# Kernel tuning notes

Hardware: AMD Instinct MI355X
Metric: run time of the kernel (lower is better)

## Reference

```python
import jax, jax.numpy as jnp
import numpy as np

D = 512
E = 1024
LAMBDA_INIT = 0.05

def setup_inputs() -> dict:
    key = jax.random.key(0)
    ks = jax.random.split(key, 8)
    B, S = 4, 4096
    X = jax.random.normal(ks[0], (B, S, E), dtype=jnp.float32)
    Wq = jax.random.normal(ks[1], (2 * D, E), dtype=jnp.float32) / np.sqrt(E)
    bq = jnp.zeros((2 * D,), dtype=jnp.float32)
    Wk = jax.random.normal(ks[2], (2 * D, E), dtype=jnp.float32) / np.sqrt(E)
    bk = jnp.zeros((2 * D,), dtype=jnp.float32)
    Wv = jax.random.normal(ks[3], (D, E), dtype=jnp.float32) / np.sqrt(E)
    bv = jnp.zeros((D,), dtype=jnp.float32)
    lam = jax.random.normal(ks[4], (1,), dtype=jnp.float32)
    return {"X": X, "Wq": Wq, "bq": bq, "Wk": Wk, "bk": bk, "Wv": Wv, "bv": bv, "lam": lam}

def reference(X, Wq, bq, Wk, bk, Wv, bv, lam):
    # Linear projections (torch Linear: x @ W.T + b)
    Q = jnp.einsum('bse,fe->bsf', X, Wq) + bq   # [B,S,2d]
    K = jnp.einsum('bse,fe->bsf', X, Wk) + bk   # [B,S,2d]
    V = jnp.einsum('bse,de->bsd', X, Wv) + bv   # [B,S,d]
    Q1, Q2 = Q[..., :D], Q[..., D:]
    K1, K2 = K[..., :D], K[..., D:]
    s = 1.0 / np.sqrt(D)
    A1 = jnp.einsum('bqd,bkd->bqk', Q1, K1) * s  # [B,S,S]
    A2 = jnp.einsum('bqd,bkd->bqk', Q2, K2) * s
    P1 = jax.nn.softmax(A1, axis=-1)
    P2 = jax.nn.softmax(A2, axis=-1)
    lambda_ = jnp.exp(lam) + LAMBDA_INIT         # scalar [1]
    diff = P1 - lambda_ * P2
    return jnp.einsum('bqk,bkd->bqd', diff, V)   # [B,S,d]
```

## Files before the change

kernel.cpp:

```cpp
#include <hip/hip_runtime.h>
#include <cstdint>
#include <cstddef>

#define NB    4
#define SEQ   4096
#define EDIM  1024
#define DHEAD 512
#define NTOK  (NB * SEQ)
#define FQK   2048
#define FQKV  2560

typedef __bf16 bf16x8 __attribute__((ext_vector_type(8)));
typedef float  f32x4  __attribute__((ext_vector_type(4)));

__device__ __forceinline__ unsigned short f2bf(float f) {
  union { float f; unsigned int u; } v; v.f = f;
  return (unsigned short)((v.u + 0x7fffu + ((v.u >> 16) & 1u)) >> 16);
}
__device__ __forceinline__ float bf2f(unsigned short h) {
  union { unsigned int u; float f; } v; v.u = ((unsigned int)h) << 16;
  return v.f;
}

__device__ __forceinline__ void gld_lds16(const void* g, void* l) {
  __builtin_amdgcn_global_load_lds(
      (const __attribute__((address_space(1))) unsigned int*)g,
      (__attribute__((address_space(3))) unsigned int*)l, 16, 0, 0);
}

template <class Epi>
__device__ __forceinline__ void gemm_bt_core(
    const unsigned short* __restrict__ A, const unsigned short* __restrict__ B,
    int K, int lda, int ldb, int m0, int n0, Epi epi) {
  __shared__ __align__(16) unsigned short As[2][128 * 32];
  __shared__ __align__(16) unsigned short Bs[2][128 * 32];
  const int t = threadIdx.x;
  const int w = t >> 6;
  const int lane = t & 63;
  const int wr = w >> 1, wc = w & 1;

  f32x4 acc[4][4];
#pragma unroll
  for (int i = 0; i < 4; ++i)
#pragma unroll
    for (int j = 0; j < 4; ++j) acc[i][j] = f32x4{0.f, 0.f, 0.f, 0.f};

  const int c0 = (w * 2) * 64 + lane;
  const int c1 = (w * 2 + 1) * 64 + lane;
  const int r0 = c0 >> 2, col0 = (c0 & 3) * 8;
  const int r1 = c1 >> 2, col1 = (c1 & 3) * 8;
  const int o0 = (w * 2) * 512;
  const int o1 = (w * 2 + 1) * 512;
  const unsigned short* gA0 = A + (size_t)(m0 + r0) * lda + col0;
  const unsigned short* gA1 = A + (size_t)(m0 + r1) * lda + col1;
  const unsigned short* gB0 = B + (size_t)(n0 + r0) * ldb + col0;
  const unsigned short* gB1 = B + (size_t)(n0 + r1) * ldb + col1;

  gld_lds16(gA0, &As[0][o0]);
  gld_lds16(gA1, &As[0][o1]);
  gld_lds16(gB0, &Bs[0][o0]);
  gld_lds16(gB1, &Bs[0][o1]);
  __syncthreads();

  int cur = 0;
  for (int kt = 0; kt < K; kt += 32) {
    const int nxt = cur ^ 1;
    if (kt + 32 < K) {
      gld_lds16(gA0 + kt + 32, &As[nxt][o0]);
      gld_lds16(gA1 + kt + 32, &As[nxt][o1]);
      gld_lds16(gB0 + kt + 32, &Bs[nxt][o0]);
      gld_lds16(gB1 + kt + 32, &Bs[nxt][o1]);
    }
    bf16x8 af[4], bfr[4];
#pragma unroll
    for (int tm = 0; tm < 4; ++tm) {
      int r = wr * 64 + tm * 16 + (lane & 15);
      af[tm] = *(const bf16x8*)&As[cur][r * 32 + (lane >> 4) * 8];
    }
#pragma unroll
    for (int tn = 0; tn < 4; ++tn) {
      int r = wc * 64 + tn * 16 + (lane & 15);
      bfr[tn] = *(const bf16x8*)&Bs[cur][r * 32 + (lane >> 4) * 8];
    }
#pragma unroll
    for (int tm = 0; tm < 4; ++tm)
#pragma unroll
      for (int tn = 0; tn < 4; ++tn)
        acc[tm][tn] = __builtin_amdgcn_mfma_f32_16x16x32_bf16(
            af[tm], bfr[tn], acc[tm][tn], 0, 0, 0);
    __syncthreads();
    cur = nxt;
  }
  epi(acc, wr, wc, lane);
}

__global__ void k_cvt_x(const float* __restrict__ X, unsigned short* __restrict__ Xb) {
  int i = blockIdx.x * blockDim.x + threadIdx.x;
  float4 v = ((const float4*)X)[i];
  ushort4 o;
  o.x = f2bf(v.x); o.y = f2bf(v.y); o.z = f2bf(v.z); o.w = f2bf(v.w);
  ((ushort4*)Xb)[i] = o;
}

__global__ void k_pack_w(const float* __restrict__ Wq, const float* __restrict__ Wk,
                         const float* __restrict__ Wv, unsigned short* __restrict__ Wb) {
  int i = blockIdx.x * blockDim.x + threadIdx.x;
  int idx = i * 4;
  int f = idx >> 10, e = idx & 1023;
  const float* src = (f < 1024) ? (Wq + (size_t)f * 1024)
                   : (f < 2048) ? (Wk + (size_t)(f - 1024) * 1024)
                                : (Wv + (size_t)(f - 2048) * 1024);
  float4 v = *(const float4*)(src + e);
  ushort4 o;
  o.x = f2bf(v.x); o.y = f2bf(v.y); o.z = f2bf(v.z); o.w = f2bf(v.w);
  ((ushort4*)Wb)[i] = o;
}

__global__ void k_pack_b(const float* __restrict__ bq, const float* __restrict__ bk,
                         const float* __restrict__ bv, float* __restrict__ bc) {
  int f = blockIdx.x * blockDim.x + threadIdx.x;
  if (f < FQKV)
    bc[f] = (f < 1024) ? bq[f] : (f < 2048) ? bk[f - 1024] : bv[f - 2048];
}

__global__ void k_zero_f(float* __restrict__ p) {
  int i = blockIdx.x * blockDim.x + threadIdx.x;
  p[i] = 0.f;
}

__global__ __launch_bounds__(256) void k_qk(const unsigned short* __restrict__ Xb,
                                            const unsigned short* __restrict__ Wb,
                                            const float* __restrict__ bc,
                                            unsigned short* __restrict__ QK) {
  const int m0 = blockIdx.y * 128, n0 = blockIdx.x * 128;
  gemm_bt_core(Xb, Wb, EDIM, EDIM, EDIM, m0, n0,
    [&](f32x4 (&acc)[4][4], int wr, int wc, int lane) {
#pragma unroll
      for (int tm = 0; tm < 4; ++tm)
#pragma unroll
        for (int tn = 0; tn < 4; ++tn) {
          int kc = n0 + wc * 64 + tn * 16 + (lane & 15);
          float bias = bc[kc];
#pragma unroll
          for (int i = 0; i < 4; ++i) {
            int q = m0 + wr * 64 + tm * 16 + (lane >> 4) * 4 + i;
            QK[(size_t)q * FQK + kc] = f2bf(acc[tm][tn][i] + bias);
          }
        }
    });
}

__global__ __launch_bounds__(256) void k_v(const unsigned short* __restrict__ Xb,
                                           const unsigned short* __restrict__ Wb,
                                           const float* __restrict__ bc,
                                           unsigned short* __restrict__ Vt) {
  const int b = blockIdx.z;
  const int m0 = blockIdx.y * 128;
  const int n0 = blockIdx.x * 128;
  const unsigned short* A = Wb + (size_t)2048 * EDIM;
  const unsigned short* B = Xb + (size_t)b * SEQ * EDIM;
  unsigned short* Vb = Vt + (size_t)b * DHEAD * SEQ;
  gemm_bt_core(A, B, EDIM, EDIM, EDIM, m0, n0,
    [&](f32x4 (&acc)[4][4], int wr, int wc, int lane) {
#pragma unroll
      for (int tm = 0; tm < 4; ++tm)
#pragma unroll
        for (int tn = 0; tn < 4; ++tn) {
          int s = n0 + wc * 64 + tn * 16 + (lane & 15);
#pragma unroll
          for (int i = 0; i < 4; ++i) {
            int d = m0 + wr * 64 + tm * 16 + (lane >> 4) * 4 + i;
            Vb[(size_t)d * SEQ + s] = f2bf(acc[tm][tn][i] + bc[2048 + d]);
          }
        }
    });
}

__global__ __launch_bounds__(512) void k_scores3(const unsigned short* __restrict__ QK,
                                                 unsigned short* __restrict__ E_c,
                                                 float* __restrict__ ls, int b0) {
  __shared__ __align__(16) unsigned short As[2][256 * 32];
  __shared__ __align__(16) unsigned short Bs[2][128 * 32];
  const int z = blockIdx.z;
  const int rb = z >> 1, which = z & 1;
  const int b = b0 + rb;
  const int m0 = blockIdx.y * 256;
  const int n0 = blockIdx.x * 128;
  const unsigned short* Aq = QK + (size_t)b * SEQ * FQK + which * 512;
  const unsigned short* Bk = QK + (size_t)b * SEQ * FQK + 1024 + which * 512;
  unsigned short* Eb = E_c + (size_t)z * SEQ * SEQ;
  float* lr = ls + (size_t)which * NTOK + (size_t)b * SEQ;
  const int t = threadIdx.x, w = t >> 6, lane = t & 63;
  const int wr = w >> 1, wc = w & 1;

  f32x4 acc[4][4];
#pragma unroll
  for (int i = 0; i < 4; ++i)
#pragma unroll
    for (int j = 0; j < 4; ++j) acc[i][j] = f32x4{0.f, 0.f, 0.f, 0.f};

  const int cA0 = w * 128 + lane;
  const int cA1 = w * 128 + 64 + lane;
  const int cB  = w * 64 + lane;
  const unsigned short* gA0 = Aq + (size_t)(m0 + (cA0 >> 2)) * FQK + (cA0 & 3) * 8;
  const unsigned short* gA1 = Aq + (size_t)(m0 + (cA1 >> 2)) * FQK + (cA1 & 3) * 8;
  const unsigned short* gB  = Bk + (size_t)(n0 + (cB >> 2)) * FQK + (cB & 3) * 8;
  const int oA0 = (w * 128) * 8;
  const int oA1 = (w * 128 + 64) * 8;
  const int oB  = (w * 64) * 8;

  gld_lds16(gA0, &As[0][oA0]);
  gld_lds16(gA1, &As[0][oA1]);
  gld_lds16(gB,  &Bs[0][oB]);
  __syncthreads();

  int cur = 0;
  for (int kt = 0; kt < 512; kt += 32) {
    const int nxt = cur ^ 1;
    if (kt + 32 < 512) {
      gld_lds16(gA0 + kt + 32, &As[nxt][oA0]);
      gld_lds16(gA1 + kt + 32, &As[nxt][oA1]);
      gld_lds16(gB + kt + 32,  &Bs[nxt][oB]);
    }
    bf16x8 af[4], bfr[4];
#pragma unroll
    for (int tm = 0; tm < 4; ++tm) {
      int r = wr * 64 + tm * 16 + (lane & 15);
      af[tm] = *(const bf16x8*)&As[cur][r * 32 + (lane >> 4) * 8];
    }
#pragma unroll
    for (int tn = 0; tn < 4; ++tn) {
      int r = wc * 64 + tn * 16 + (lane & 15);
      bfr[tn] = *(const bf16x8*)&Bs[cur][r * 32 + (lane >> 4) * 8];
    }
#pragma unroll
    for (int tm = 0; tm < 4; ++tm)
#pragma unroll
      for (int tn = 0; tn < 4; ++tn)
        acc[tm][tn] = __builtin_amdgcn_mfma_f32_16x16x32_bf16(
            af[tm], bfr[tn], acc[tm][tn], 0, 0, 0);
    __syncthreads();
    cur = nxt;
  }

  const float scale = 0.04419417382415922f;
  float rs[4][4];
#pragma unroll
  for (int tm = 0; tm < 4; ++tm)
#pragma unroll
    for (int i = 0; i < 4; ++i) rs[tm][i] = 0.f;
#pragma unroll
  for (int tm = 0; tm < 4; ++tm)
#pragma unroll
    for (int tn = 0; tn < 4; ++tn) {
      int k = n0 + wc * 64 + tn * 16 + (lane & 15);
#pragma unroll
      for (int i = 0; i < 4; ++i) {
        int q = m0 + wr * 64 + tm * 16 + (lane >> 4) * 4 + i;
        float e = __expf(acc[tm][tn][i] * scale);
        unsigned short eb = f2bf(e);
        Eb[(size_t)q * SEQ + k] = eb;
        rs[tm][i] += bf2f(eb);
      }
    }
#pragma unroll
  for (int tm = 0; tm < 4; ++tm)
#pragma unroll
    for (int i = 0; i < 4; ++i) {
      float v = rs[tm][i];
      v += __shfl_xor(v, 1);
      v += __shfl_xor(v, 2);
      v += __shfl_xor(v, 4);
      v += __shfl_xor(v, 8);
      rs[tm][i] = v;
    }
  if ((lane & 15) == 0) {
#pragma unroll
    for (int tm = 0; tm < 4; ++tm)
#pragma unroll
      for (int i = 0; i < 4; ++i) {
        int q = m0 + wr * 64 + tm * 16 + (lane >> 4) * 4 + i;
        atomicAdd(&lr[q], rs[tm][i]);
      }
  }
}

__global__ __launch_bounds__(256) void k_pv4(const unsigned short* __restrict__ E_c,
                                             const unsigned short* __restrict__ Vt,
                                             float* __restrict__ O12, int b0) {
  __shared__ __align__(16) unsigned short As[2][64 * 32];
  __shared__ __align__(16) unsigned short Bs[2][256 * 32];
  const int bid = blockIdx.x;
  const int z = (bid >> 1) & 3;
  const int e = (bid & 1) | ((bid >> 3) << 1);
  const int q0 = (e >> 1) * 64;
  const int n0 = (e & 1) * 256;
  const int b = b0 + (z >> 1);
  const unsigned short* A = E_c + (size_t)z * SEQ * SEQ;
  const unsigned short* Bv = Vt + (size_t)b * DHEAD * SEQ;
  float* Ob = O12 + (size_t)z * SEQ * DHEAD;
  const int t = threadIdx.x, w = t >> 6, lane = t & 63;

  f32x4 acc[4][4];
#pragma unroll
  for (int i = 0; i < 4; ++i)
#pragma unroll
    for (int j = 0; j < 4; ++j) acc[i][j] = f32x4{0.f, 0.f, 0.f, 0.f};

  const int ca = w * 64 + lane;
  const unsigned short* gA = A + (size_t)(q0 + (ca >> 2)) * SEQ + (ca & 3) * 8;
  const int oA = (w * 64) * 8;
  const unsigned short* gB[4];
  int oB[4];
#pragma unroll
  for (int g = 0; g < 4; ++g) {
    int c = w * 256 + g * 64 + lane;
    gB[g] = Bv + (size_t)(n0 + (c >> 2)) * SEQ + (c & 3) * 8;
    oB[g] = (w * 256 + g * 64) * 8;
  }

  gld_lds16(gA, &As[0][oA]);
#pragma unroll
  for (int g = 0; g < 4; ++g) gld_lds16(gB[g], &Bs[0][oB[g]]);
  __syncthreads();

  int cur = 0;
  for (int kt = 0; kt < SEQ; kt += 32) {
    const int nxt = cur ^ 1;
    if (kt + 32 < SEQ) {
      gld_lds16(gA + kt + 32, &As[nxt][oA]);
#pragma unroll
      for (int g = 0; g < 4; ++g) gld_lds16(gB[g] + kt + 32, &Bs[nxt][oB[g]]);
    }
    bf16x8 af[4], bfr[4];
#pragma unroll
    for (int tm = 0; tm < 4; ++tm) {
      int r = tm * 16 + (lane & 15);
      af[tm] = *(const bf16x8*)&As[cur][r * 32 + (lane >> 4) * 8];
    }
#pragma unroll
    for (int tn = 0; tn < 4; ++tn) {
      int r = w * 64 + tn * 16 + (lane & 15);
      bfr[tn] = *(const bf16x8*)&Bs[cur][r * 32 + (lane >> 4) * 8];
    }
#pragma unroll
    for (int tm = 0; tm < 4; ++tm)
#pragma unroll
      for (int tn = 0; tn < 4; ++tn)
        acc[tm][tn] = __builtin_amdgcn_mfma_f32_16x16x32_bf16(
            af[tm], bfr[tn], acc[tm][tn], 0, 0, 0);
    __syncthreads();
    cur = nxt;
  }

#pragma unroll
  for (int tm = 0; tm < 4; ++tm)
#pragma unroll
    for (int tn = 0; tn < 4; ++tn) {
      int d = n0 + w * 64 + tn * 16 + (lane & 15);
#pragma unroll
      for (int i = 0; i < 4; ++i) {
        int q = q0 + tm * 16 + (lane >> 4) * 4 + i;
        Ob[(size_t)q * DHEAD + d] = acc[tm][tn][i];
      }
    }
}

__global__ void k_combine(const float* __restrict__ O12, const float* __restrict__ ls,
                          const float* __restrict__ lam, float* __restrict__ out, int b0) {
  int i = blockIdx.x * blockDim.x + threadIdx.x;
  float lambda = expf(lam[0]) + 0.05f;
  int gq = i >> 7;
  int rb = gq >> 12;
  int q = gq & 4095;
  int dv = i & 127;
  int b = b0 + rb;
  float inv1 = 1.f / ls[(size_t)b * SEQ + q];
  float inv2 = lambda / ls[NTOK + (size_t)b * SEQ + q];
  size_t ai = (size_t)(rb * 2) * (SEQ * 128) + (size_t)q * 128 + dv;
  float4 a = ((const float4*)O12)[ai];
  float4 c = ((const float4*)O12)[ai + SEQ * 128];
  float4 r;
  r.x = a.x * inv1 - c.x * inv2;
  r.y = a.y * inv1 - c.y * inv2;
  r.z = a.z * inv1 - c.z * inv2;
  r.w = a.w * inv1 - c.w * inv2;
  ((float4*)out)[(size_t)(b * SEQ + q) * 128 + dv] = r;
}

extern "C" void kernel_launch(void* const* d_in, const int* in_sizes, int n_in,
                              void* d_out, int out_size, void* d_ws, size_t ws_size,
                              hipStream_t stream) {
  const float* X   = (const float*)d_in[0];
  const float* Wq  = (const float*)d_in[1];
  const float* bq  = (const float*)d_in[2];
  const float* Wk  = (const float*)d_in[3];
  const float* bk  = (const float*)d_in[4];
  const float* Wv  = (const float*)d_in[5];
  const float* bv  = (const float*)d_in[6];
  const float* lam = (const float*)d_in[7];
  float* out = (float*)d_out;

  char* ws = (char*)d_ws;
  size_t off = 0;
  auto alloc = [&](size_t b) { size_t r = off; off += (b + 255) & ~(size_t)255; return r; };
  unsigned short* Xb  = (unsigned short*)(ws + alloc((size_t)NTOK * EDIM * 2));
  unsigned short* Wb  = (unsigned short*)(ws + alloc((size_t)FQKV * EDIM * 2));
  float*          bc  = (float*)(ws + alloc((size_t)FQKV * 4));
  unsigned short* QK  = (unsigned short*)(ws + alloc((size_t)NTOK * FQK * 2));
  unsigned short* Vt  = (unsigned short*)(ws + alloc((size_t)NB * DHEAD * SEQ * 2));
  unsigned short* E_c = (unsigned short*)(ws + alloc((size_t)4 * SEQ * SEQ * 2));
  float*          ls  = (float*)(ws + alloc((size_t)2 * NTOK * 4));
  float* O12 = (float*)Xb;

  k_cvt_x<<<dim3((NTOK * EDIM / 4) / 256), dim3(256), 0, stream>>>(X, Xb);
  k_pack_w<<<dim3((FQKV * EDIM / 4) / 256), dim3(256), 0, stream>>>(Wq, Wk, Wv, Wb);
  k_pack_b<<<dim3(10), dim3(256), 0, stream>>>(bq, bk, bv, bc);
  k_qk<<<dim3(FQK / 128, NTOK / 128), dim3(256), 0, stream>>>(Xb, Wb, bc, QK);
  k_v<<<dim3(SEQ / 128, DHEAD / 128, NB), dim3(256), 0, stream>>>(Xb, Wb, bc, Vt);
  k_zero_f<<<dim3(2 * NTOK / 256), dim3(256), 0, stream>>>(ls);
  for (int b0 = 0; b0 < NB; b0 += 2) {
    k_scores3<<<dim3(SEQ / 128, SEQ / 256, 4), dim3(512), 0, stream>>>(QK, E_c, ls, b0);
    k_pv4<<<dim3(512), dim3(256), 0, stream>>>(E_c, Vt, O12, b0);
    k_combine<<<dim3((2 * SEQ * DHEAD / 4) / 256), dim3(256), 0, stream>>>(O12, ls, lam, out, b0);
  }

  (void)in_sizes; (void)n_in; (void)out_size; (void)ws_size;
}
```

Baseline: 719.9 us.

## Triple-buffer LDS staging with partial vmcnt waits in all GEMM kernels

Moves the three GEMM-style kernels (generic projection GEMM, scores, PV) from double to triple buffering of their LDS tiles. Global-to-LDS loads are issued two tiles ahead, and each step waits only on the older tile's loads through an explicit s_waitcnt vmcnt(N) and a raw barrier instead of a full __syncthreads. The goal is to keep more memory traffic in flight and hide load latency behind MFMA work. The cost is 1.5x LDS per block, which may reduce occupancy, and a reliance on hand-counted vmcnt values being correct.

```diff
diff --git a/kernel.cpp b/kernel.cpp
--- a/kernel.cpp
+++ b/kernel.cpp
@@ -13,6 +13,9 @@
 typedef __bf16 bf16x8 __attribute__((ext_vector_type(8)));
 typedef float  f32x4  __attribute__((ext_vector_type(4)));
 
+#define WAITCNT(VM) asm volatile("s_waitcnt vmcnt(" #VM ") lgkmcnt(0)" ::: "memory")
+#define BAR() __builtin_amdgcn_s_barrier()
+
 __device__ __forceinline__ unsigned short f2bf(float f) {
   union { float f; unsigned int u; } v; v.f = f;
   return (unsigned short)((v.u + 0x7fffu + ((v.u >> 16) & 1u)) >> 16);
@@ -32,8 +35,8 @@
 __device__ __forceinline__ void gemm_bt_core(
     const unsigned short* __restrict__ A, const unsigned short* __restrict__ B,
     int K, int lda, int ldb, int m0, int n0, Epi epi) {
-  __shared__ __align__(16) unsigned short As[2][128 * 32];
-  __shared__ __align__(16) unsigned short Bs[2][128 * 32];
+  __shared__ __align__(16) unsigned short As[3][128 * 32];
+  __shared__ __align__(16) unsigned short Bs[3][128 * 32];
   const int t = threadIdx.x;
   const int w = t >> 6;
   const int lane = t & 63;
@@ -56,20 +59,25 @@
   const unsigned short* gB0 = B + (size_t)(n0 + r0) * ldb + col0;
   const unsigned short* gB1 = B + (size_t)(n0 + r1) * ldb + col1;
 
-  gld_lds16(gA0, &As[0][o0]);
-  gld_lds16(gA1, &As[0][o1]);
-  gld_lds16(gB0, &Bs[0][o0]);
-  gld_lds16(gB1, &Bs[0][o1]);
-  __syncthreads();
+  auto stage = [&](int buf, int tt) {
+    const int kt = tt * 32;
+    gld_lds16(gA0 + kt, &As[buf][o0]);
+    gld_lds16(gA1 + kt, &As[buf][o1]);
+    gld_lds16(gB0 + kt, &Bs[buf][o0]);
+    gld_lds16(gB1 + kt, &Bs[buf][o1]);
+  };
+
+  const int NT = K >> 5;
+  stage(0, 0);
+  stage(1, 1);
+  WAITCNT(4);
+  BAR();
 
   int cur = 0;
-  for (int kt = 0; kt < K; kt += 32) {
-    const int nxt = cur ^ 1;
-    if (kt + 32 < K) {
-      gld_lds16(gA0 + kt + 32, &As[nxt][o0]);
-      gld_lds16(gA1 + kt + 32, &As[nxt][o1]);
-      gld_lds16(gB0 + kt + 32, &Bs[nxt][o0]);
-      gld_lds16(gB1 + kt + 32, &Bs[nxt][o1]);
+  for (int tt = 0; tt < NT; ++tt) {
+    if (tt + 2 < NT) {
+      const int sb = (cur >= 1) ? cur - 1 : 2;
+      stage(sb, tt + 2);
     }
     bf16x8 af[4], bfr[4];
 #pragma unroll
@@ -88,8 +96,9 @@
       for (int tn = 0; tn < 4; ++tn)
         acc[tm][tn] = __builtin_amdgcn_mfma_f32_16x16x32_bf16(
             af[tm], bfr[tn], acc[tm][tn], 0, 0, 0);
-    __syncthreads();
-    cur = nxt;
+    if (tt < NT - 2)       { WAITCNT(4); BAR(); }
+    else if (tt == NT - 2) { WAITCNT(0); BAR(); }
+    cur = (cur == 2) ? 0 : cur + 1;
   }
   epi(acc, wr, wc, lane);
 }
@@ -179,8 +188,8 @@
 __global__ __launch_bounds__(512) void k_scores3(const unsigned short* __restrict__ QK,
                                                  unsigned short* __restrict__ E_c,
                                                  float* __restrict__ ls, int b0) {
-  __shared__ __align__(16) unsigned short As[2][256 * 32];
-  __shared__ __align__(16) unsigned short Bs[2][128 * 32];
+  __shared__ __align__(16) unsigned short As[3][256 * 32];
+  __shared__ __align__(16) unsigned short Bs[3][128 * 32];
   const int z = blockIdx.z;
   const int rb = z >> 1, which = z & 1;
   const int b = b0 + rb;
@@ -209,18 +218,24 @@
   const int oA1 = (w * 128 + 64) * 8;
   const int oB  = (w * 64) * 8;
 
-  gld_lds16(gA0, &As[0][oA0]);
-  gld_lds16(gA1, &As[0][oA1]);
-  gld_lds16(gB,  &Bs[0][oB]);
-  __syncthreads();
+  auto stage = [&](int buf, int tt) {
+    const int kt = tt * 32;
+    gld_lds16(gA0 + kt, &As[buf][oA0]);
+    gld_lds16(gA1 + kt, &As[buf][oA1]);
+    gld_lds16(gB + kt,  &Bs[buf][oB]);
+  };
+
+  const int NT = 16;
+  stage(0, 0);
+  stage(1, 1);
+  WAITCNT(3);
+  BAR();
 
   int cur = 0;
-  for (int kt = 0; kt < 512; kt += 32) {
-    const int nxt = cur ^ 1;
-    if (kt + 32 < 512) {
-      gld_lds16(gA0 + kt + 32, &As[nxt][oA0]);
-      gld_lds16(gA1 + kt + 32, &As[nxt][oA1]);
-      gld_lds16(gB + kt + 32,  &Bs[nxt][oB]);
+  for (int tt = 0; tt < NT; ++tt) {
+    if (tt + 2 < NT) {
+      const int sb = (cur >= 1) ? cur - 1 : 2;
+      stage(sb, tt + 2);
     }
     bf16x8 af[4], bfr[4];
 #pragma unroll
@@ -239,8 +254,9 @@
       for (int tn = 0; tn < 4; ++tn)
         acc[tm][tn] = __builtin_amdgcn_mfma_f32_16x16x32_bf16(
             af[tm], bfr[tn], acc[tm][tn], 0, 0, 0);
-    __syncthreads();
-    cur = nxt;
+    if (tt < NT - 2)       { WAITCNT(3); BAR(); }
+    else if (tt == NT - 2) { WAITCNT(0); BAR(); }
+    cur = (cur == 2) ? 0 : cur + 1;
   }
 
   const float scale = 0.04419417382415922f;
@@ -288,8 +304,8 @@
 __global__ __launch_bounds__(256) void k_pv4(const unsigned short* __restrict__ E_c,
                                              const unsigned short* __restrict__ Vt,
                                              float* __restrict__ O12, int b0) {
-  __shared__ __align__(16) unsigned short As[2][64 * 32];
-  __shared__ __align__(16) unsigned short Bs[2][256 * 32];
+  __shared__ __align__(16) unsigned short As[3][64 * 32];
+  __shared__ __align__(16) unsigned short Bs[3][256 * 32];
   const int bid = blockIdx.x;
   const int z = (bid >> 1) & 3;
   const int e = (bid & 1) | ((bid >> 3) << 1);
@@ -319,18 +335,24 @@
     oB[g] = (w * 256 + g * 64) * 8;
   }
 
-  gld_lds16(gA, &As[0][oA]);
-#pragma unroll
-  for (int g = 0; g < 4; ++g) gld_lds16(gB[g], &Bs[0][oB[g]]);
-  __syncthreads();
+  auto stage = [&](int buf, int tt) {
+    const int kt = tt * 32;
+    gld_lds16(gA + kt, &As[buf][oA]);
+#pragma unroll
+    for (int g = 0; g < 4; ++g) gld_lds16(gB[g] + kt, &Bs[buf][oB[g]]);
+  };
+
+  const int NT = SEQ / 32;
+  stage(0, 0);
+  stage(1, 1);
+  WAITCNT(5);
+  BAR();
 
   int cur = 0;
-  for (int kt = 0; kt < SEQ; kt += 32) {
-    const int nxt = cur ^ 1;
-    if (kt + 32 < SEQ) {
-      gld_lds16(gA + kt + 32, &As[nxt][oA]);
-#pragma unroll
-      for (int g = 0; g < 4; ++g) gld_lds16(gB[g] + kt + 32, &Bs[nxt][oB[g]]);
+  for (int tt = 0; tt < NT; ++tt) {
+    if (tt + 2 < NT) {
+      const int sb = (cur >= 1) ? cur - 1 : 2;
+      stage(sb, tt + 2);
     }
     bf16x8 af[4], bfr[4];
 #pragma unroll
@@ -349,8 +371,9 @@
       for (int tn = 0; tn < 4; ++tn)
         acc[tm][tn] = __builtin_amdgcn_mfma_f32_16x16x32_bf16(
             af[tm], bfr[tn], acc[tm][tn], 0, 0, 0);
-    __syncthreads();
-    cur = nxt;
+    if (tt < NT - 2)       { WAITCNT(5); BAR(); }
+    else if (tt == NT - 2) { WAITCNT(0); BAR(); }
+    cur = (cur == 2) ? 0 : cur + 1;
   }
 
 #pragma unroll
```

Result: slower. 807.1 us (+12.1%).

## Enlarge score and PV GEMM tiles with XOR-swizzled LDS and K=64 stages

Applied to the files above, without the earlier changes.

Both the score GEMM and the PV GEMM now use larger 256-wide tiles, 512 threads and a K step of 64 per LDS stage. Stage columns are XOR-swizzled to avoid LDS bank conflicts, and s_setprio raises wave priority around the MFMA section. PV blocks move from 64x256 to 256x128 tiles on a 3D grid, which changes how much E and V each block reuses. The cost is more LDS and registers per block (launch bounds 512,2), which may reduce occupancy.

```diff
diff --git a/kernel.cpp b/kernel.cpp
--- a/kernel.cpp
+++ b/kernel.cpp
@@ -176,87 +176,95 @@
     });
 }
 
-__global__ __launch_bounds__(512) void k_scores3(const unsigned short* __restrict__ QK,
-                                                 unsigned short* __restrict__ E_c,
-                                                 float* __restrict__ ls, int b0) {
-  __shared__ __align__(16) unsigned short As[2][256 * 32];
-  __shared__ __align__(16) unsigned short Bs[2][128 * 32];
-  const int z = blockIdx.z;
-  const int rb = z >> 1, which = z & 1;
-  const int b = b0 + rb;
-  const int m0 = blockIdx.y * 256;
-  const int n0 = blockIdx.x * 128;
+__global__ __launch_bounds__(512, 2) void k_scores8(const unsigned short* __restrict__ QK,
+                                                    unsigned short* __restrict__ E_c,
+                                                    float* __restrict__ ls, int b0) {
+  __shared__ __align__(16) unsigned short LA[2][256 * 64];
+  __shared__ __align__(16) unsigned short LB[2][256 * 64];
+  const int z = blockIdx.z, rb = z >> 1, which = z & 1, b = b0 + rb;
+  const int m0 = blockIdx.y * 256, n0 = blockIdx.x * 256;
   const unsigned short* Aq = QK + (size_t)b * SEQ * FQK + which * 512;
-  const unsigned short* Bk = QK + (size_t)b * SEQ * FQK + 1024 + which * 512;
+  const unsigned short* Bk = Aq + 1024;
   unsigned short* Eb = E_c + (size_t)z * SEQ * SEQ;
   float* lr = ls + (size_t)which * NTOK + (size_t)b * SEQ;
   const int t = threadIdx.x, w = t >> 6, lane = t & 63;
-  const int wr = w >> 1, wc = w & 1;
-
-  f32x4 acc[4][4];
-#pragma unroll
-  for (int i = 0; i < 4; ++i)
+  const int wr = w >> 2, wc = w & 3;
+  const int l15 = lane & 15, c16 = lane >> 4, x7 = l15 & 7;
+
+  f32x4 acc[8][4];
+#pragma unroll
+  for (int i = 0; i < 8; ++i)
 #pragma unroll
     for (int j = 0; j < 4; ++j) acc[i][j] = f32x4{0.f, 0.f, 0.f, 0.f};
 
-  const int cA0 = w * 128 + lane;
-  const int cA1 = w * 128 + 64 + lane;
-  const int cB  = w * 64 + lane;
-  const unsigned short* gA0 = Aq + (size_t)(m0 + (cA0 >> 2)) * FQK + (cA0 & 3) * 8;
-  const unsigned short* gA1 = Aq + (size_t)(m0 + (cA1 >> 2)) * FQK + (cA1 & 3) * 8;
-  const unsigned short* gB  = Bk + (size_t)(n0 + (cB >> 2)) * FQK + (cB & 3) * 8;
-  const int oA0 = (w * 128) * 8;
-  const int oA1 = (w * 128 + 64) * 8;
-  const int oB  = (w * 64) * 8;
-
-  gld_lds16(gA0, &As[0][oA0]);
-  gld_lds16(gA1, &As[0][oA1]);
-  gld_lds16(gB,  &Bs[0][oB]);
+  unsigned goffA[4], goffB[4]; int loff[4];
+#pragma unroll
+  for (int i = 0; i < 4; ++i) {
+    int c = w * 64 + lane + 512 * i;
+    int r = c >> 3;
+    int sg = (c & 7) ^ (r & 7);
+    goffA[i] = (unsigned)((m0 + r) * FQK + sg * 8);
+    goffB[i] = (unsigned)((n0 + r) * FQK + sg * 8);
+    loff[i] = (w * 64 + 512 * i) * 8;
+  }
+
+  auto STAGE = [&](int buf, int kh) {
+#pragma unroll
+    for (int i = 0; i < 4; ++i) gld_lds16(Aq + goffA[i] + kh, &LA[buf][loff[i]]);
+#pragma unroll
+    for (int i = 0; i < 4; ++i) gld_lds16(Bk + goffB[i] + kh, &LB[buf][loff[i]]);
+  };
+
+  STAGE(0, 0);
   __syncthreads();
 
-  int cur = 0;
-  for (int kt = 0; kt < 512; kt += 32) {
-    const int nxt = cur ^ 1;
-    if (kt + 32 < 512) {
-      gld_lds16(gA0 + kt + 32, &As[nxt][oA0]);
-      gld_lds16(gA1 + kt + 32, &As[nxt][oA1]);
-      gld_lds16(gB + kt + 32,  &Bs[nxt][oB]);
-    }
-    bf16x8 af[4], bfr[4];
-#pragma unroll
-    for (int tm = 0; tm < 4; ++tm) {
-      int r = wr * 64 + tm * 16 + (lane & 15);
-      af[tm] = *(const bf16x8*)&As[cur][r * 32 + (lane >> 4) * 8];
-    }
+  for (int kt = 0; kt < 8; ++kt) {
+    const int cb = kt & 1;
+    if (kt < 7) STAGE(cb ^ 1, (kt + 1) * 64);
+    __builtin_amdgcn_s_setprio(1);
+    bf16x8 bfr[4][2];
+#pragma unroll
+    for (int tn = 0; tn < 4; ++tn)
+#pragma unroll
+      for (int ks = 0; ks < 2; ++ks)
+        bfr[tn][ks] = *(const bf16x8*)
+            &LB[cb][(wc * 64 + tn * 16 + l15) * 64 + (((ks * 4 + c16) ^ x7) * 8)];
+#pragma unroll
+    for (int mh = 0; mh < 2; ++mh) {
+      bf16x8 af[4][2];
+#pragma unroll
+      for (int tq = 0; tq < 4; ++tq)
+#pragma unroll
+        for (int ks = 0; ks < 2; ++ks)
+          af[tq][ks] = *(const bf16x8*)
+              &LA[cb][(wr * 128 + mh * 64 + tq * 16 + l15) * 64 + (((ks * 4 + c16) ^ x7) * 8)];
+#pragma unroll
+      for (int tq = 0; tq < 4; ++tq)
+#pragma unroll
+        for (int tn = 0; tn < 4; ++tn)
+#pragma unroll
+          for (int ks = 0; ks < 2; ++ks)
+            acc[mh * 4 + tq][tn] = __builtin_amdgcn_mfma_f32_16x16x32_bf16(
+                af[tq][ks], bfr[tn][ks], acc[mh * 4 + tq][tn], 0, 0, 0);
+    }
+    __builtin_amdgcn_s_setprio(0);
+    __syncthreads();
+  }
+
+  const float scale = 0.04419417382415922f;
+  float rs[8][4];
+#pragma unroll
+  for (int tm = 0; tm < 8; ++tm)
+#pragma unroll
+    for (int i = 0; i < 4; ++i) rs[tm][i] = 0.f;
+#pragma unroll
+  for (int tm = 0; tm < 8; ++tm)
 #pragma unroll
     for (int tn = 0; tn < 4; ++tn) {
-      int r = wc * 64 + tn * 16 + (lane & 15);
-      bfr[tn] = *(const bf16x8*)&Bs[cur][r * 32 + (lane >> 4) * 8];
-    }
-#pragma unroll
-    for (int tm = 0; tm < 4; ++tm)
-#pragma unroll
-      for (int tn = 0; tn < 4; ++tn)
-        acc[tm][tn] = __builtin_amdgcn_mfma_f32_16x16x32_bf16(
-            af[tm], bfr[tn], acc[tm][tn], 0, 0, 0);
-    __syncthreads();
-    cur = nxt;
-  }
-
-  const float scale = 0.04419417382415922f;
-  float rs[4][4];
-#pragma unroll
-  for (int tm = 0; tm < 4; ++tm)
-#pragma unroll
-    for (int i = 0; i < 4; ++i) rs[tm][i] = 0.f;
-#pragma unroll
-  for (int tm = 0; tm < 4; ++tm)
-#pragma unroll
-    for (int tn = 0; tn < 4; ++tn) {
-      int k = n0 + wc * 64 + tn * 16 + (lane & 15);
+      int k = n0 + wc * 64 + tn * 16 + l15;
 #pragma unroll
       for (int i = 0; i < 4; ++i) {
-        int q = m0 + wr * 64 + tm * 16 + (lane >> 4) * 4 + i;
+        int q = m0 + wr * 128 + tm * 16 + c16 * 4 + i;
         float e = __expf(acc[tm][tn][i] * scale);
         unsigned short eb = f2bf(e);
         Eb[(size_t)q * SEQ + k] = eb;
@@ -264,7 +272,7 @@
       }
     }
 #pragma unroll
-  for (int tm = 0; tm < 4; ++tm)
+  for (int tm = 0; tm < 8; ++tm)
 #pragma unroll
     for (int i = 0; i < 4; ++i) {
       float v = rs[tm][i];
@@ -274,32 +282,30 @@
       v += __shfl_xor(v, 8);
       rs[tm][i] = v;
     }
-  if ((lane & 15) == 0) {
-#pragma unroll
-    for (int tm = 0; tm < 4; ++tm)
+  if (l15 == 0) {
+#pragma unroll
+    for (int tm = 0; tm < 8; ++tm)
 #pragma unroll
       for (int i = 0; i < 4; ++i) {
-        int q = m0 + wr * 64 + tm * 16 + (lane >> 4) * 4 + i;
+        int q = m0 + wr * 128 + tm * 16 + c16 * 4 + i;
         atomicAdd(&lr[q], rs[tm][i]);
       }
   }
 }
 
-__global__ __launch_bounds__(256) void k_pv4(const unsigned short* __restrict__ E_c,
-                                             const unsigned short* __restrict__ Vt,
-                                             float* __restrict__ O12, int b0) {
-  __shared__ __align__(16) unsigned short As[2][64 * 32];
-  __shared__ __align__(16) unsigned short Bs[2][256 * 32];
-  const int bid = blockIdx.x;
-  const int z = (bid >> 1) & 3;
-  const int e = (bid & 1) | ((bid >> 3) << 1);
-  const int q0 = (e >> 1) * 64;
-  const int n0 = (e & 1) * 256;
-  const int b = b0 + (z >> 1);
-  const unsigned short* A = E_c + (size_t)z * SEQ * SEQ;
+__global__ __launch_bounds__(512, 2) void k_pv8(const unsigned short* __restrict__ E_c,
+                                                const unsigned short* __restrict__ Vt,
+                                                float* __restrict__ O12, int b0) {
+  __shared__ __align__(16) unsigned short LA[2][256 * 64];
+  __shared__ __align__(16) unsigned short LB[2][128 * 64];
+  const int z = blockIdx.z, b = b0 + (z >> 1);
+  const int q0 = blockIdx.y * 256, n0 = blockIdx.x * 128;
+  const unsigned short* Ae = E_c + (size_t)z * SEQ * SEQ;
   const unsigned short* Bv = Vt + (size_t)b * DHEAD * SEQ;
   float* Ob = O12 + (size_t)z * SEQ * DHEAD;
   const int t = threadIdx.x, w = t >> 6, lane = t & 63;
+  const int wr = w >> 1, wc = w & 1;
+  const int l15 = lane & 15, c16 = lane >> 4, x7 = l15 & 7;
 
   f32x4 acc[4][4];
 #pragma unroll
@@ -307,61 +313,72 @@
 #pragma unroll
     for (int j = 0; j < 4; ++j) acc[i][j] = f32x4{0.f, 0.f, 0.f, 0.f};
 
-  const int ca = w * 64 + lane;
-  const unsigned short* gA = A + (size_t)(q0 + (ca >> 2)) * SEQ + (ca & 3) * 8;
-  const int oA = (w * 64) * 8;
-  const unsigned short* gB[4];
-  int oB[4];
-#pragma unroll
-  for (int g = 0; g < 4; ++g) {
-    int c = w * 256 + g * 64 + lane;
-    gB[g] = Bv + (size_t)(n0 + (c >> 2)) * SEQ + (c & 3) * 8;
-    oB[g] = (w * 256 + g * 64) * 8;
-  }
-
-  gld_lds16(gA, &As[0][oA]);
-#pragma unroll
-  for (int g = 0; g < 4; ++g) gld_lds16(gB[g], &Bs[0][oB[g]]);
+  unsigned goffE[4], goffV[2]; int loffE[4], loffV[2];
+#pragma unroll
+  for (int i = 0; i < 4; ++i) {
+    int c = w * 64 + lane + 512 * i;
+    int r = c >> 3;
+    int sg = (c & 7) ^ (r & 7);
+    goffE[i] = (unsigned)((q0 + r) * SEQ + sg * 8);
+    loffE[i] = (w * 64 + 512 * i) * 8;
+  }
+#pragma unroll
+  for (int i = 0; i < 2; ++i) {
+    int c = w * 64 + lane + 512 * i;
+    int r = c >> 3;
+    int sg = (c & 7) ^ (r & 7);
+    goffV[i] = (unsigned)((n0 + r) * SEQ + sg * 8);
+    loffV[i] = (w * 64 + 512 * i) * 8;
+  }
+
+  auto STAGE = [&](int buf, int kh) {
+#pragma unroll
+    for (int i = 0; i < 4; ++i) gld_lds16(Ae + goffE[i] + kh, &LA[buf][loffE[i]]);
+#pragma unroll
+    for (int i = 0; i < 2; ++i) gld_lds16(Bv + goffV[i] + kh, &LB[buf][loffV[i]]);
+  };
+
+  STAGE(0, 0);
   __syncthreads();
 
-  int cur = 0;
-  for (int kt = 0; kt < SEQ; kt += 32) {
-    const int nxt = cur ^ 1;
-    if (kt + 32 < SEQ) {
-      gld_lds16(gA + kt + 32, &As[nxt][oA]);
-#pragma unroll
-      for (int g = 0; g < 4; ++g) gld_lds16(gB[g] + kt + 32, &Bs[nxt][oB[g]]);
-    }
-    bf16x8 af[4], bfr[4];
-#pragma unroll
-    for (int tm = 0; tm < 4; ++tm) {
-      int r = tm * 16 + (lane & 15);
-      af[tm] = *(const bf16x8*)&As[cur][r * 32 + (lane >> 4) * 8];
-    }
+  for (int kt = 0; kt < 64; ++kt) {
+    const int cb = kt & 1;
+    if (kt < 63) STAGE(cb ^ 1, (kt + 1) * 64);
+    __builtin_amdgcn_s_setprio(1);
+    bf16x8 af[4][2], bfr[4][2];
+#pragma unroll
+    for (int tn = 0; tn < 4; ++tn)
+#pragma unroll
+      for (int ks = 0; ks < 2; ++ks)
+        bfr[tn][ks] = *(const bf16x8*)
+            &LB[cb][(wc * 64 + tn * 16 + l15) * 64 + (((ks * 4 + c16) ^ x7) * 8)];
+#pragma unroll
+    for (int tq = 0; tq < 4; ++tq)
+#pragma unroll
+      for (int ks = 0; ks < 2; ++ks)
+        af[tq][ks] = *(const bf16x8*)
+            &LA[cb][(wr * 64 + tq * 16 + l15) * 64 + (((ks * 4 + c16) ^ x7) * 8)];
+#pragma unroll
+    for (int tq = 0; tq < 4; ++tq)
+#pragma unroll
+      for (int tn = 0; tn < 4; ++tn)
+#pragma unroll
+        for (int ks = 0; ks < 2; ++ks)
+          acc[tq][tn] = __builtin_amdgcn_mfma_f32_16x16x32_bf16(
+              af[tq][ks], bfr[tn][ks], acc[tq][tn], 0, 0, 0);
+    __builtin_amdgcn_s_setprio(0);
+    __syncthreads();
+  }
+
+#pragma unroll
+  for (int tq = 0; tq < 4; ++tq)
 #pragma unroll
     for (int tn = 0; tn < 4; ++tn) {
-      int r = w * 64 + tn * 16 + (lane & 15);
-      bfr[tn] = *(const bf16x8*)&Bs[cur][r * 32 + (lane >> 4) * 8];
-    }
-#pragma unroll
-    for (int tm = 0; tm < 4; ++tm)
-#pragma unroll
-      for (int tn = 0; tn < 4; ++tn)
-        acc[tm][tn] = __builtin_amdgcn_mfma_f32_16x16x32_bf16(
-            af[tm], bfr[tn], acc[tm][tn], 0, 0, 0);
-    __syncthreads();
-    cur = nxt;
-  }
-
-#pragma unroll
-  for (int tm = 0; tm < 4; ++tm)
-#pragma unroll
-    for (int tn = 0; tn < 4; ++tn) {
-      int d = n0 + w * 64 + tn * 16 + (lane & 15);
+      int d = n0 + wc * 64 + tn * 16 + l15;
 #pragma unroll
       for (int i = 0; i < 4; ++i) {
-        int q = q0 + tm * 16 + (lane >> 4) * 4 + i;
-        Ob[(size_t)q * DHEAD + d] = acc[tm][tn][i];
+        int q = q0 + wr * 64 + tq * 16 + c16 * 4 + i;
+        Ob[(size_t)q * DHEAD + d] = acc[tq][tn][i];
       }
     }
 }
@@ -420,8 +437,8 @@
   k_v<<<dim3(SEQ / 128, DHEAD / 128, NB), dim3(256), 0, stream>>>(Xb, Wb, bc, Vt);
   k_zero_f<<<dim3(2 * NTOK / 256), dim3(256), 0, stream>>>(ls);
   for (int b0 = 0; b0 < NB; b0 += 2) {
-    k_scores3<<<dim3(SEQ / 128, SEQ / 256, 4), dim3(512), 0, stream>>>(QK, E_c, ls, b0);
-    k_pv4<<<dim3(512), dim3(256), 0, stream>>>(E_c, Vt, O12, b0);
+    k_scores8<<<dim3(SEQ / 256, SEQ / 256, 4), dim3(512), 0, stream>>>(QK, E_c, ls, b0);
+    k_pv8<<<dim3(DHEAD / 128, SEQ / 256, 4), dim3(512), 0, stream>>>(E_c, Vt, O12, b0);
     k_combine<<<dim3((2 * SEQ * DHEAD / 4) / 256), dim3(256), 0, stream>>>(O12, ls, lam, out, b0);
   }
 
```

Result: faster. 689.3 us (-4.2%).
